# Optimization experiments

Hardware: AMD Instinct MI355X
Metric: run time of the kernel (lower is better)

Reference implementation:

```python
import jax, jax.numpy as jnp
import numpy as np

B, N, C_ATT, H, L = 4, 2048, 256, 8, 2
TOPK = 32        # torch.topk k (only index 0 per channel is used)
NSAMPLE = 32     # max_radius_points
RADIUS = 0.3
EPS = 1e-5


def _bn(x, g, b, axes):
    # training-mode batch norm (biased variance), channel dim = 1
    m = jnp.mean(x, axes, keepdims=True)
    v = jnp.var(x, axes, keepdims=True)
    sh = [1] * x.ndim
    sh[1] = -1
    return (x - m) / jnp.sqrt(v + EPS) * g.reshape(sh) + b.reshape(sh)


def _ln(x, g, b):
    m = jnp.mean(x, -1, keepdims=True)
    v = jnp.var(x, -1, keepdims=True)
    return (x - m) / jnp.sqrt(v + EPS) * g + b


def setup_inputs() -> dict:
    key = jax.random.key(0)
    ks = iter(jax.random.split(key, 40))
    def w(shape, fan):
        return jax.random.normal(next(ks), shape, jnp.float32) / np.sqrt(fan)
    return {
        "hoch_features": jax.random.normal(next(ks), (B, C_ATT, N), jnp.float32),
        "pts": jax.random.uniform(next(ks), (B, 3, N), jnp.float32),
        "Wq": w((L, C_ATT, C_ATT), C_ATT), "Wk": w((L, C_ATT, C_ATT), C_ATT),
        "Wv": w((L, C_ATT, C_ATT), C_ATT), "Wo": w((L, C_ATT, C_ATT), C_ATT),
        "ln_g": jnp.ones((L, C_ATT)), "ln_b": jnp.zeros((L, C_ATT)),
        "fg_w1": w((64, C_ATT), C_ATT), "fg_b1": jnp.zeros((64,)),
        "fg_w2": w((32, 64), 64), "fg_b2": jnp.zeros((32,)),
        "fg_w3": w((16, 32), 32), "fg_b3": jnp.zeros((16,)),
        "fg_g1": jnp.ones((64,)), "fg_be1": jnp.zeros((64,)),
        "fg_g2": jnp.ones((32,)), "fg_be2": jnp.zeros((32,)),
        "fg_g3": jnp.ones((16,)), "fg_be3": jnp.zeros((16,)),
        "cw1": w((64, 3), 3), "cw2": w((256, 64), 64), "cw3": w((512, 256), 256),
        "cg1": jnp.ones((64,)), "cb1": jnp.zeros((64,)),
        "cg2": jnp.ones((256,)), "cb2": jnp.zeros((256,)),
        "cg3": jnp.ones((512,)), "cb3": jnp.zeros((512,)),
    }


def _forward(hoch_features, pts, Wq, Wk, Wv, Wo, ln_g, ln_b,
             fg_w1, fg_b1, fg_w2, fg_b2, fg_w3, fg_b3,
             fg_g1, fg_be1, fg_g2, fg_be2, fg_g3, fg_be3,
             cw1, cw2, cw3, cg1, cb1, cg2, cb2, cg3, cb3):
    # ---- multi-head self-attention stack on (B,N,C) ----
    x = hoch_features.transpose(0, 2, 1)
    dh = C_ATT // H
    for l in range(L):
        q = (x @ Wq[l]).reshape(B, N, H, dh)
        k = (x @ Wk[l]).reshape(B, N, H, dh)
        v = (x @ Wv[l]).reshape(B, N, H, dh)
        att = jax.nn.softmax(jnp.einsum('bnhd,bmhd->bhnm', q, k) / np.sqrt(dh).astype(np.float32))
        o = jnp.einsum('bhnm,bmhd->bnhd', att, v).reshape(B, N, C_ATT) @ Wo[l]
        x = _ln(x + o, ln_g[l], ln_b[l])
    feats = x.transpose(0, 2, 1)                      # (B,256,N)
    # ---- feat_generator: 1x1 conv1d -> BN -> relu chain 256->64->32->16 ----
    h = jax.nn.relu(_bn(jnp.einsum('oc,bcn->bon', fg_w1, feats) + fg_b1[:, None], fg_g1, fg_be1, (0, 2)))
    h = jax.nn.relu(_bn(jnp.einsum('oc,bcn->bon', fg_w2, h) + fg_b2[:, None], fg_g2, fg_be2, (0, 2)))
    h = jax.nn.relu(_bn(jnp.einsum('oc,bcn->bon', fg_w3, h) + fg_b3[:, None], fg_g3, fg_be3, (0, 2)))  # (B,16,N)
    # ---- topk over points, keep argmax per channel -> 16 query points ----
    _, ti = jax.lax.top_k(h, TOPK)                    # (B,16,32)
    idx = ti[:, :, 0]                                 # (B,16)
    all_pts = pts.transpose(0, 2, 1)                  # (B,N,3)
    qpts = jax.vmap(lambda p, i: p[i])(all_pts, idx)  # (B,16,3)
    # ---- ball query (fixed-radius kNN fill, PointNet++ style) ----
    sqd = (jnp.sum(qpts * qpts, -1)[:, :, None] + jnp.sum(all_pts * all_pts, -1)[:, None, :]
           - 2.0 * jnp.einsum('bsc,bnc->bsn', qpts, all_pts))      # (B,16,N)
    gi = jnp.broadcast_to(jnp.arange(N), sqd.shape)
    gi = jnp.where(sqd > RADIUS * RADIUS, N, gi)
    gi = jnp.sort(gi, axis=-1)[:, :, :NSAMPLE]
    gi = jnp.where(gi == N, gi[:, :, :1], gi)         # (B,16,32)
    rpts = jax.vmap(lambda p, i: p[i])(all_pts, gi)   # (B,16,32,3)
    grouped = jnp.concatenate([qpts[:, :, None, :], rpts], axis=2)  # (B,16,33,3)
    g = grouped.transpose(0, 3, 1, 2)                 # (B,3,16,33)
    # ---- 1x1 conv2d -> BN2d -> LeakyReLU(0.2) chain 3->64->256->512 ----
    lrelu = lambda t: jnp.where(t > 0, t, 0.2 * t)
    g = lrelu(_bn(jnp.einsum('oc,bcsk->bosk', cw1, g), cg1, cb1, (0, 2, 3)))
    g = lrelu(_bn(jnp.einsum('oc,bcsk->bosk', cw2, g), cg2, cb2, (0, 2, 3)))
    g = lrelu(_bn(jnp.einsum('oc,bcsk->bosk', cw3, g), cg3, cb3, (0, 2, 3)))
    return jnp.max(g, axis=-1)                        # (B,512,16)


def reference(hoch_features, pts, Wq, Wk, Wv, Wo, ln_g, ln_b,
              fg_w1, fg_b1, fg_w2, fg_b2, fg_w3, fg_b3,
              fg_g1, fg_be1, fg_g2, fg_be2, fg_g3, fg_be3,
              cw1, cw2, cw3, cg1, cb1, cg2, cb2, cg3, cb3):
    return _forward(hoch_features, pts, Wq, Wk, Wv, Wo, ln_g, ln_b,
                    fg_w1, fg_b1, fg_w2, fg_b2, fg_w3, fg_b3,
                    fg_g1, fg_be1, fg_g2, fg_be2, fg_g3, fg_be3,
                    cw1, cw2, cw3, cg1, cb1, cg2, cb2, cg3, cb3)
```

## Files before the change

### kernel.cpp

```cpp
#include <hip/hip_runtime.h>
#include <hip/hip_bf16.h>
#include <math.h>

#define BB 4
#define NN 2048
#define CC 256
#define HH 8
#define DH 32
#define LL 2
#define SS 16
#define KK 33
#define NSAMPLE 32
#define EPSV 1e-5f

typedef _Float16 f16x8 __attribute__((ext_vector_type(8)));
typedef _Float16 f16x4 __attribute__((ext_vector_type(4)));
typedef float f32x4 __attribute__((ext_vector_type(4)));

struct hl16 { _Float16 h, l; };
__device__ __forceinline__ hl16 split2(float v) {
    hl16 r;
    r.h = (_Float16)v;
    r.l = (_Float16)(v - (float)r.h);
    return r;
}

#define INV_MF (1.f / 8192.f)
#define INV_MG (1.f / 2112.f)

#define WT_SLOT 65536
#define FG1H_OFF 1048576
#define FG1L_OFF (FG1H_OFF + 16384)
#define CW2H_OFF (FG1H_OFF + 32768)
#define CW2L_OFF (FG1H_OFF + 49152)
#define CW3H_OFF (FG1H_OFF + 65536)
#define CW3L_OFF (CW3H_OFF + 131072)

__global__ __launch_bounds__(256) void prep_split_k(
    const float* __restrict__ Wq, const float* __restrict__ Wk,
    const float* __restrict__ Wv, const float* __restrict__ Wo,
    const float* __restrict__ fgw1, const float* __restrict__ cw2,
    const float* __restrict__ cw3, _Float16* __restrict__ wt,
    float* __restrict__ stats0) {
    int e = blockIdx.x * 256 + threadIdx.x;
    if (e < 6144) stats0[e] = 0.f;
    if (e < 524288) {
        int slot = e >> 16;
        int l = slot >> 2, mat = slot & 3;
        int r = e & 65535;
        int n = r >> 8, k = r & 255;
        const float* W = mat == 0 ? Wq : mat == 1 ? Wk : mat == 2 ? Wv : Wo;
        hl16 s = split2(W[(size_t)l * 65536 + k * 256 + n]);
        wt[(size_t)(2 * slot) * WT_SLOT + n * 256 + k] = s.h;
        wt[(size_t)(2 * slot + 1) * WT_SLOT + n * 256 + k] = s.l;
    } else if (e < 524288 + 16384) {
        int r = e - 524288;
        hl16 s = split2(fgw1[r]);
        wt[FG1H_OFF + r] = s.h;
        wt[FG1L_OFF + r] = s.l;
    } else if (e < 524288 + 32768) {
        int r = e - (524288 + 16384);
        hl16 s = split2(cw2[r]);
        wt[CW2H_OFF + r] = s.h;
        wt[CW2L_OFF + r] = s.l;
    } else if (e < 524288 + 32768 + 131072) {
        int r = e - (524288 + 32768);
        hl16 s = split2(cw3[r]);
        wt[CW3H_OFF + r] = s.h;
        wt[CW3L_OFF + r] = s.l;
    }
}

__global__ __launch_bounds__(256) void transpose_split_k(const float* __restrict__ in,
                                                         float* __restrict__ out,
                                                         _Float16* __restrict__ oh,
                                                         _Float16* __restrict__ ol) {
    __shared__ float tls[32][33];
    int n0 = blockIdx.x * 32, c0 = blockIdx.y * 32, b = blockIdx.z;
    const float* ip = in + (size_t)b * CC * NN;
    size_t ob = (size_t)b * NN * CC;
    int tx = threadIdx.x, ty = threadIdx.y;
#pragma unroll
    for (int i = 0; i < 4; ++i)
        tls[ty + i * 8][tx] = ip[(size_t)(c0 + ty + i * 8) * NN + n0 + tx];
    __syncthreads();
#pragma unroll
    for (int i = 0; i < 4; ++i) {
        size_t oi = ob + (size_t)(n0 + ty + i * 8) * CC + c0 + tx;
        float v = tls[tx][ty + i * 8];
        out[oi] = v;
        hl16 s = split2(v);
        oh[oi] = s.h;
        ol[oi] = s.l;
    }
}

template <bool TRANSB, bool BIAS>
__global__ __launch_bounds__(256) void gemm_k(const float* __restrict__ A,
                                              const float* __restrict__ Bm,
                                              const float* __restrict__ bias,
                                              float* __restrict__ Cm,
                                              int M, int Nc, int K,
                                              const float* __restrict__ pst,
                                              const float* __restrict__ pg,
                                              const float* __restrict__ pb,
                                              float pInvM,
                                              float* __restrict__ ost) {
    __shared__ float As[16][68];
    __shared__ float Bs[16][68];
    __shared__ float sSc[64], sSh[64];
    int t = threadIdx.x;
    int tx = t & 15, ty = t >> 4;
    int row0 = blockIdx.y * 64, col0 = blockIdx.x * 64;
    if (pst && t < K) {
        float mean = pst[t] * pInvM;
        float var = pst[K + t] * pInvM - mean * mean;
        float wv = rsqrtf(var + EPSV) * pg[t];
        sSc[t] = wv;
        sSh[t] = pb[t] - mean * wv;
    }
    if (pst) __syncthreads();
    float acc[4][4] = {};
    for (int k0 = 0; k0 < K; k0 += 16) {
#pragma unroll
        for (int p = 0; p < 4; ++p) {
            int i = t + 256 * p;
            int m = i >> 4, k = i & 15;
            int gm = row0 + m, gk = k0 + k;
            float av = 0.f;
            if (gm < M && gk < K) {
                av = A[(size_t)gm * K + gk];
                if (pst) {
                    av = fmaf(av, sSc[gk], sSh[gk]);
                    av = fmaxf(av, 0.f);
                }
            }
            As[k][m] = av;
        }
#pragma unroll
        for (int p = 0; p < 4; ++p) {
            int i = t + 256 * p;
            if (TRANSB) {
                int k = i & 15, n = i >> 4;
                int gn = col0 + n, gk = k0 + k;
                Bs[k][n] = (gn < Nc && gk < K) ? Bm[(size_t)gn * K + gk] : 0.f;
            } else {
                int n = i & 63, k = i >> 6;
                int gn = col0 + n, gk = k0 + k;
                Bs[k][n] = (gn < Nc && gk < K) ? Bm[(size_t)gk * Nc + gn] : 0.f;
            }
        }
        __syncthreads();
#pragma unroll
        for (int kk = 0; kk < 16; ++kk) {
            float4 a4 = *(const float4*)&As[kk][ty * 4];
            float4 b4 = *(const float4*)&Bs[kk][tx * 4];
            float av[4] = {a4.x, a4.y, a4.z, a4.w};
            float bv[4] = {b4.x, b4.y, b4.z, b4.w};
#pragma unroll
            for (int i = 0; i < 4; ++i)
#pragma unroll
                for (int j = 0; j < 4; ++j) acc[i][j] = fmaf(av[i], bv[j], acc[i][j]);
        }
        __syncthreads();
    }
    float cs[4] = {}, css[4] = {};
#pragma unroll
    for (int i = 0; i < 4; ++i) {
        int r = row0 + ty * 4 + i;
        if (r >= M) continue;
#pragma unroll
        for (int j = 0; j < 4; ++j) {
            int c = col0 + tx * 4 + j;
            if (c >= Nc) continue;
            float v = acc[i][j];
            if (BIAS) v += bias[c];
            Cm[(size_t)r * Nc + c] = v;
            cs[j] += v;
            css[j] += v * v;
        }
    }
    if (ost) {
        float* sc = &As[0][0];
        if (t < 128) sc[t] = 0.f;
        __syncthreads();
#pragma unroll
        for (int j = 0; j < 4; ++j) {
            atomicAdd(&sc[tx * 4 + j], cs[j]);
            atomicAdd(&sc[64 + tx * 4 + j], css[j]);
        }
        __syncthreads();
        if (t < Nc) atomicAdd(&ost[t], sc[t]);
        else if (t >= 64 && t - 64 < Nc) atomicAdd(&ost[Nc + t - 64], sc[t]);
    }
}

#define EPI_F32 0
#define EPI_QK 1
#define EPI_VT 2

template <int TM>
__device__ __forceinline__ void gemm_h_body(
    const _Float16* __restrict__ Ah, const _Float16* __restrict__ Al,
    const _Float16* __restrict__ Bh, const _Float16* __restrict__ Bl,
    const float* __restrict__ bias, float* __restrict__ Cf,
    _Float16* __restrict__ Ch, _Float16* __restrict__ Cl,
    int Nc, int K, int row0, int col0, int mode, float scl,
    float* __restrict__ ost,
    _Float16* sAh, _Float16* sAl, _Float16* sBh, _Float16* sBl) {
    int t = threadIdx.x, w = t >> 6, lane = t & 63;
    int col = lane & 15, quad = lane >> 4;
    const int m0w = (TM == 128) ? (w & 1) * 64 : 0;
    const int n0w = (TM == 128) ? (w >> 1) * 32 : w * 16;
    constexpr int NT = (TM == 128) ? 2 : 1;
    constexpr int AC = TM / 64;
    f32x4 acc[4][NT];
#pragma unroll
    for (int i = 0; i < 4; ++i)
#pragma unroll
        for (int j = 0; j < NT; ++j) acc[i][j] = (f32x4){0.f, 0.f, 0.f, 0.f};

    for (int k0 = 0; k0 < K; k0 += 32) {
        f16x8 rah[AC], ral[AC], rbh, rbl;
#pragma unroll
        for (int i = 0; i < AC; ++i) {
            int idx = t + 256 * i;
            int r = idx >> 2, off = (idx & 3) * 8;
            rah[i] = *(const f16x8*)(Ah + (size_t)(row0 + r) * K + k0 + off);
            ral[i] = *(const f16x8*)(Al + (size_t)(row0 + r) * K + k0 + off);
        }
        {
            int r = t >> 2, off = (t & 3) * 8;
            rbh = *(const f16x8*)(Bh + (size_t)(col0 + r) * K + k0 + off);
            rbl = *(const f16x8*)(Bl + (size_t)(col0 + r) * K + k0 + off);
        }
        __syncthreads();
#pragma unroll
        for (int i = 0; i < AC; ++i) {
            int idx = t + 256 * i;
            int r = idx >> 2, off = (idx & 3) * 8;
            *(f16x8*)&sAh[r * 40 + off] = rah[i];
            *(f16x8*)&sAl[r * 40 + off] = ral[i];
        }
        {
            int r = t >> 2, off = (t & 3) * 8;
            *(f16x8*)&sBh[r * 40 + off] = rbh;
            *(f16x8*)&sBl[r * 40 + off] = rbl;
        }
        __syncthreads();
        f16x8 fah[4], fal[4], fbh[NT], fbl[NT];
#pragma unroll
        for (int i = 0; i < 4; ++i) {
            fah[i] = *(const f16x8*)&sAh[(m0w + i * 16 + col) * 40 + quad * 8];
            fal[i] = *(const f16x8*)&sAl[(m0w + i * 16 + col) * 40 + quad * 8];
        }
#pragma unroll
        for (int j = 0; j < NT; ++j) {
            fbh[j] = *(const f16x8*)&sBh[(n0w + j * 16 + col) * 40 + quad * 8];
            fbl[j] = *(const f16x8*)&sBl[(n0w + j * 16 + col) * 40 + quad * 8];
        }
#pragma unroll
        for (int i = 0; i < 4; ++i)
#pragma unroll
            for (int j = 0; j < NT; ++j) {
                acc[i][j] = __builtin_amdgcn_mfma_f32_16x16x32_f16(fah[i], fbh[j], acc[i][j], 0, 0, 0);
                acc[i][j] = __builtin_amdgcn_mfma_f32_16x16x32_f16(fah[i], fbl[j], acc[i][j], 0, 0, 0);
                acc[i][j] = __builtin_amdgcn_mfma_f32_16x16x32_f16(fal[i], fbh[j], acc[i][j], 0, 0, 0);
            }
    }
    float s = 0.f, ss = 0.f;
#pragma unroll
    for (int i = 0; i < 4; ++i)
#pragma unroll
        for (int j = 0; j < NT; ++j) {
            int n = col0 + n0w + j * 16 + col;
            int mb = row0 + m0w + i * 16 + quad * 4;
            if (mode == EPI_F32) {
                float bv = bias ? bias[n] : 0.f;
#pragma unroll
                for (int r = 0; r < 4; ++r) {
                    float v = acc[i][j][r] + bv;
                    Cf[(size_t)(mb + r) * Nc + n] = v;
                    s += v;
                    ss += v * v;
                }
            } else if (mode == EPI_QK) {
#pragma unroll
                for (int r = 0; r < 4; ++r) {
                    hl16 sp = split2(acc[i][j][r] * scl);
                    Ch[(size_t)(mb + r) * Nc + n] = sp.h;
                    Cl[(size_t)(mb + r) * Nc + n] = sp.l;
                }
            } else {
                int b = mb >> 11, token = mb & 2047;
                int h = n >> 5, d = n & 31;
                f16x4 h4, l4;
#pragma unroll
                for (int r = 0; r < 4; ++r) {
                    hl16 sp = split2(acc[i][j][r]);
                    h4[r] = sp.h;
                    l4[r] = sp.l;
                }
                size_t dst = ((size_t)(b * HH + h) * DH + d) * NN + token;
                *(f16x4*)&Ch[dst] = h4;
                *(f16x4*)&Cl[dst] = l4;
            }
        }
    if (ost && mode == EPI_F32 && TM == 64) {
        s += __shfl_xor(s, 16);
        s += __shfl_xor(s, 32);
        ss += __shfl_xor(ss, 16);
        ss += __shfl_xor(ss, 32);
        if (quad == 0) {
            int n = col0 + n0w + col;
            atomicAdd(&ost[n], s);
            atomicAdd(&ost[Nc + n], ss);
        }
    }
}

template <int TM>
__global__ __launch_bounds__(256) void gemm_h_k(const _Float16* __restrict__ Ah,
                                                const _Float16* __restrict__ Al,
                                                const _Float16* __restrict__ Bh,
                                                const _Float16* __restrict__ Bl,
                                                const float* __restrict__ bias,
                                                float* __restrict__ Cf, int Nc, int K,
                                                float* __restrict__ ost) {
    __shared__ _Float16 sAh[TM * 40], sAl[TM * 40], sBh[64 * 40], sBl[64 * 40];
    gemm_h_body<TM>(Ah, Al, Bh, Bl, bias, Cf, nullptr, nullptr, Nc, K,
                    blockIdx.y * TM, blockIdx.x * 64, EPI_F32, 1.f, ost,
                    sAh, sAl, sBh, sBl);
}

__global__ __launch_bounds__(256) void qkv_h_k(const _Float16* __restrict__ Xh,
                                               const _Float16* __restrict__ Xl,
                                               const _Float16* __restrict__ wt, int layer,
                                               _Float16* Qh, _Float16* Ql,
                                               _Float16* Kh, _Float16* Kl,
                                               _Float16* Vh, _Float16* Vl) {
    __shared__ _Float16 sAh[128 * 40], sAl[128 * 40], sBh[64 * 40], sBl[64 * 40];
    int mat = blockIdx.x >> 2;
    int slot = (layer * 4 + mat) * 2;
    const _Float16* Bh = wt + (size_t)slot * WT_SLOT;
    const _Float16* Bl = wt + (size_t)(slot + 1) * WT_SLOT;
    _Float16* Ch = mat == 0 ? Qh : mat == 1 ? Kh : Vh;
    _Float16* Cl = mat == 0 ? Ql : mat == 1 ? Kl : Vl;
    int mode = (mat == 2) ? EPI_VT : EPI_QK;
    float scl = (mat == 0) ? 0.25501654859214384f : 1.f;
    gemm_h_body<128>(Xh, Xl, Bh, Bl, nullptr, nullptr, Ch, Cl, CC, CC,
                     blockIdx.y * 128, (blockIdx.x & 3) * 64, mode, scl, nullptr,
                     sAh, sAl, sBh, sBl);
}

__global__ __launch_bounds__(256) void attn6_k(const _Float16* __restrict__ Qhp,
                                               const _Float16* __restrict__ Qlp,
                                               const _Float16* __restrict__ Kh,
                                               const _Float16* __restrict__ Kl,
                                               const _Float16* __restrict__ Vh,
                                               const _Float16* __restrict__ Vl,
                                               float* __restrict__ O0,
                                               float* __restrict__ O1,
                                               float* __restrict__ ML) {
    __shared__ _Float16 sKh[64 * 40], sKl[64 * 40];
    __shared__ _Float16 sVh[32 * 72], sVl[32 * 72];
    __shared__ _Float16 sPh[4][16 * 40], sPl[4][16 * 40];
    int t = threadIdx.x, w = t >> 6, lane = t & 63;
    int col = lane & 15, quad = lane >> 4;
    int bh = blockIdx.z, b = bh >> 3, h = bh & 7;
    int kh = blockIdx.y;
    int qbase = blockIdx.x * 64 + w * 16;

    size_t qoff = ((size_t)(b * NN + qbase + col)) * CC + h * DH + quad * 8;
    f16x8 qh = *(const f16x8*)(Qhp + qoff);
    f16x8 ql = *(const f16x8*)(Qlp + qoff);

    f32x4 o0 = {0.f, 0.f, 0.f, 0.f}, o1 = {0.f, 0.f, 0.f, 0.f};
    float mrun = -1e30f, lsum = 0.f;

    const _Float16* fKh = &sKh[col * 40 + quad * 8];
    const _Float16* fKl = &sKl[col * 40 + quad * 8];
    const _Float16* fVh0 = &sVh[col * 72 + quad * 8];
    const _Float16* fVl0 = &sVl[col * 72 + quad * 8];
    const _Float16* fVh1 = &sVh[(16 + col) * 72 + quad * 8];
    const _Float16* fVl1 = &sVl[(16 + col) * 72 + quad * 8];
    _Float16* wPh = &sPh[w][col * 40 + quad * 4];
    _Float16* wPl = &sPl[w][col * 40 + quad * 4];
    const _Float16* rPh = &sPh[w][col * 40 + quad * 8];
    const _Float16* rPl = &sPl[w][col * 40 + quad * 8];

    int pidx = t & 127;
    int krow = pidx >> 1, koff = (pidx & 1) * 16;
    int vrow = pidx >> 2, voff = (pidx & 3) * 16;
    const _Float16* kg = (t < 128 ? Kh : Kl) + (size_t)b * NN * CC + h * DH;
    const _Float16* vg = (t < 128 ? Vh : Vl) + ((size_t)(b * HH + h) * DH + vrow) * NN;
    _Float16* dK = (t < 128 ? sKh : sKl) + krow * 40 + koff;
    _Float16* dV = (t < 128 ? sVh : sVl) + vrow * 72 + voff;

    int kbase = kh * (NN / 2);
    for (int k0 = kbase; k0 < kbase + NN / 2; k0 += 64) {
        const _Float16* kp = kg + (size_t)(k0 + krow) * CC + koff;
        f16x8 rk0 = *(const f16x8*)kp;
        f16x8 rk1 = *(const f16x8*)(kp + 8);
        const _Float16* vp = vg + k0 + voff;
        f16x8 rv0 = *(const f16x8*)vp;
        f16x8 rv1 = *(const f16x8*)(vp + 8);
        __syncthreads();
        *(f16x8*)dK = rk0;
        *(f16x8*)(dK + 8) = rk1;
        *(f16x8*)dV = rv0;
        *(f16x8*)(dV + 8) = rv1;
        __syncthreads();

        f32x4 s[4];
#pragma unroll
        for (int kt = 0; kt < 4; ++kt) {
            f16x8 ka = *(const f16x8*)(fKh + kt * 16 * 40);
            f16x8 kb = *(const f16x8*)(fKl + kt * 16 * 40);
            f32x4 z = {0.f, 0.f, 0.f, 0.f};
            z = __builtin_amdgcn_mfma_f32_16x16x32_f16(ka, qh, z, 0, 0, 0);
            z = __builtin_amdgcn_mfma_f32_16x16x32_f16(ka, ql, z, 0, 0, 0);
            z = __builtin_amdgcn_mfma_f32_16x16x32_f16(kb, qh, z, 0, 0, 0);
            s[kt] = z;
        }

        float tm = -1e30f;
#pragma unroll
        for (int kt = 0; kt < 4; ++kt)
#pragma unroll
            for (int r = 0; r < 4; ++r) tm = fmaxf(tm, s[kt][r]);
        tm = fmaxf(tm, __shfl_xor(tm, 16));
        tm = fmaxf(tm, __shfl_xor(tm, 32));
        float nm = fmaxf(mrun, tm);
        float alpha = __builtin_amdgcn_exp2f(mrun - nm);
        float p[16], rs = 0.f;
#pragma unroll
        for (int kt = 0; kt < 4; ++kt)
#pragma unroll
            for (int r = 0; r < 4; ++r) {
                float pv = __builtin_amdgcn_exp2f(s[kt][r] - nm);
                p[kt * 4 + r] = pv;
                rs += pv;
            }
        rs += __shfl_xor(rs, 16);
        rs += __shfl_xor(rs, 32);
        lsum = lsum * alpha + rs;
        mrun = nm;
        o0.x *= alpha; o0.y *= alpha; o0.z *= alpha; o0.w *= alpha;
        o1.x *= alpha; o1.y *= alpha; o1.z *= alpha; o1.w *= alpha;

#pragma unroll
        for (int c = 0; c < 2; ++c) {
#pragma unroll
            for (int k2 = 0; k2 < 2; ++k2) {
                int kt = c * 2 + k2;
                f16x4 h4, l4;
#pragma unroll
                for (int r = 0; r < 4; ++r) {
                    hl16 sp = split2(p[kt * 4 + r]);
                    h4[r] = sp.h;
                    l4[r] = sp.l;
                }
                *(f16x4*)(wPh + k2 * 16) = h4;
                *(f16x4*)(wPl + k2 * 16) = l4;
            }
            __asm__ volatile("s_waitcnt lgkmcnt(0)" ::: "memory");
            f16x8 pH = *(const f16x8*)rPh;
            f16x8 pL = *(const f16x8*)rPl;

            f16x8 va = *(const f16x8*)(fVh0 + c * 32);
            f16x8 vb = *(const f16x8*)(fVl0 + c * 32);
            o0 = __builtin_amdgcn_mfma_f32_16x16x32_f16(va, pH, o0, 0, 0, 0);
            o0 = __builtin_amdgcn_mfma_f32_16x16x32_f16(va, pL, o0, 0, 0, 0);
            o0 = __builtin_amdgcn_mfma_f32_16x16x32_f16(vb, pH, o0, 0, 0, 0);
            f16x8 vc = *(const f16x8*)(fVh1 + c * 32);
            f16x8 vd = *(const f16x8*)(fVl1 + c * 32);
            o1 = __builtin_amdgcn_mfma_f32_16x16x32_f16(vc, pH, o1, 0, 0, 0);
            o1 = __builtin_amdgcn_mfma_f32_16x16x32_f16(vc, pL, o1, 0, 0, 0);
            o1 = __builtin_amdgcn_mfma_f32_16x16x32_f16(vd, pH, o1, 0, 0, 0);
        }
    }

    float* OP = (kh == 0) ? O0 : O1;
    int q = qbase + col;
    size_t oi = ((size_t)bh * NN + q) * 32;
    *(f32x4*)&OP[oi + quad * 4] = o0;
    *(f32x4*)&OP[oi + 16 + quad * 4] = o1;
    if (quad == 0) {
        float2* mlp = (float2*)ML;
        mlp[(size_t)kh * (BB * HH * NN) + (size_t)bh * NN + q] = make_float2(mrun, lsum);
    }
}

__global__ __launch_bounds__(256) void attn_comb_k(const float* __restrict__ O0,
                                                   const float* __restrict__ O1,
                                                   const float* __restrict__ ML,
                                                   _Float16* __restrict__ QOh,
                                                   _Float16* __restrict__ QOl) {
    int i = blockIdx.x * 256 + threadIdx.x;
    int bh = i >> 11, q = i & 2047;
    int b = bh >> 3, h = bh & 7;
    const float2* mlp = (const float2*)ML;
    float2 ml0 = mlp[i];
    float2 ml1 = mlp[BB * HH * NN + i];
    float m = fmaxf(ml0.x, ml1.x);
    float a0 = __builtin_amdgcn_exp2f(ml0.x - m);
    float a1 = __builtin_amdgcn_exp2f(ml1.x - m);
    float inv = 1.f / (ml0.y * a0 + ml1.y * a1);
    a0 *= inv;
    a1 *= inv;
    size_t src = (size_t)i * 32;
    size_t dst = ((size_t)(b * NN + q)) * CC + h * DH;
#pragma unroll
    for (int d = 0; d < 32; d += 4) {
        float4 v0 = *(const float4*)&O0[src + d];
        float4 v1 = *(const float4*)&O1[src + d];
        float vv[4] = {v0.x * a0 + v1.x * a1, v0.y * a0 + v1.y * a1,
                       v0.z * a0 + v1.z * a1, v0.w * a0 + v1.w * a1};
        f16x4 h4, l4;
#pragma unroll
        for (int r = 0; r < 4; ++r) {
            hl16 s = split2(vv[r]);
            h4[r] = s.h;
            l4[r] = s.l;
        }
        *(f16x4*)&QOh[dst + d] = h4;
        *(f16x4*)&QOl[dst + d] = l4;
    }
}

__global__ __launch_bounds__(256) void add_ln_k(float* __restrict__ X,
                                                const float* __restrict__ P,
                                                const float* __restrict__ g,
                                                const float* __restrict__ bta,
                                                _Float16* __restrict__ Xh,
                                                _Float16* __restrict__ Xl) {
    int wave = threadIdx.x >> 6, lane = threadIdx.x & 63;
    size_t row = (size_t)blockIdx.x * 4 + wave;
    size_t base = row * CC + lane * 4;
    float4 x = *(float4*)(X + base);
    float4 p = *(const float4*)(P + base);
    x.x += p.x; x.y += p.y; x.z += p.z; x.w += p.w;
    float sum = x.x + x.y + x.z + x.w;
    float ss = x.x * x.x + x.y * x.y + x.z * x.z + x.w * x.w;
#pragma unroll
    for (int off = 32; off; off >>= 1) {
        sum += __shfl_down(sum, off);
        ss += __shfl_down(ss, off);
    }
    sum = __shfl(sum, 0);
    ss = __shfl(ss, 0);
    float mean = sum * (1.f / 256.f);
    float var = ss * (1.f / 256.f) - mean * mean;
    float wn = rsqrtf(var + EPSV);
    float4 gg = *(const float4*)(g + lane * 4);
    float4 bb = *(const float4*)(bta + lane * 4);
    x.x = (x.x - mean) * wn * gg.x + bb.x;
    x.y = (x.y - mean) * wn * gg.y + bb.y;
    x.z = (x.z - mean) * wn * gg.z + bb.z;
    x.w = (x.w - mean) * wn * gg.w + bb.w;
    *(float4*)(X + base) = x;
    f16x4 h4, l4;
    float xv[4] = {x.x, x.y, x.z, x.w};
#pragma unroll
    for (int j = 0; j < 4; ++j) {
        hl16 s = split2(xv[j]);
        h4[j] = s.h;
        l4[j] = s.l;
    }
    *(f16x4*)&Xh[base] = h4;
    *(f16x4*)&Xl[base] = l4;
}

__global__ __launch_bounds__(256) void applyc_k(const float* __restrict__ in,
                                                _Float16* __restrict__ oh,
                                                _Float16* __restrict__ ol,
                                                const float* __restrict__ st,
                                                const float* __restrict__ gam,
                                                const float* __restrict__ bet,
                                                int total, int Cc, float invM) {
    int i = blockIdx.x * 256 + threadIdx.x;
    if (i >= total) return;
    int c = i % Cc;
    float mean = st[c] * invM;
    float var = st[Cc + c] * invM - mean * mean;
    float sc = rsqrtf(var + EPSV) * gam[c];
    float v = fmaf(in[i] - mean, sc, bet[c]);
    v = v > 0.f ? v : 0.2f * v;
    hl16 s = split2(v);
    oh[i] = s.h;
    ol[i] = s.l;
}

__global__ __launch_bounds__(64) void select_k(const float* __restrict__ H3,
                                               const float* __restrict__ pts,
                                               const float* __restrict__ st,
                                               const float* __restrict__ gam,
                                               const float* __restrict__ bet,
                                               float* __restrict__ G0) {
    int bs = blockIdx.x;
    int b = bs >> 4, ch = bs & 15;
    int lane = threadIdx.x;
    float mean = st[ch] * INV_MF;
    float var = st[16 + ch] * INV_MF - mean * mean;
    float sc = rsqrtf(var + EPSV) * gam[ch];
    float sh = bet[ch] - mean * sc;
    float best = -1e30f;
    int bn = 0;
    for (int n = lane; n < NN; n += 64) {
        float v = fmaf(H3[((size_t)(b * NN + n)) * 16 + ch], sc, sh);
        v = fmaxf(v, 0.f);
        if (v > best) { best = v; bn = n; }
    }
#pragma unroll
    for (int off = 32; off; off >>= 1) {
        float ov = __shfl_xor(best, off);
        int on = __shfl_xor(bn, off);
        if (ov > best || (ov == best && on < bn)) { best = ov; bn = on; }
    }
    const float* px = pts + (size_t)b * 3 * NN;
    float qx = px[bn], qy = px[NN + bn], qz = px[2 * NN + bn];
    float qq = (qx * qx + qy * qy) + qz * qz;
    __shared__ int sgi[NSAMPLE];
    const float R2 = 0.09f;
    int cnt = 0;
    for (int base = 0; base < NN && cnt < NSAMPLE; base += 64) {
        int n = base + lane;
        float x = px[n], y = px[NN + n], z = px[2 * NN + n];
        float pp = (x * x + y * y) + z * z;
        float dot = (qx * x + qy * y) + qz * z;
        float sqd = (qq + pp) - 2.f * dot;
        bool ok = !(sqd > R2);
        unsigned long long mk = __ballot(ok);
        int pos = cnt + (int)__popcll(mk & ((1ull << lane) - 1ull));
        if (ok && pos < NSAMPLE) sgi[pos] = n;
        cnt += (int)__popcll(mk);
    }
    __syncthreads();
    int g0 = sgi[0];
    if (lane >= cnt && lane < NSAMPLE) sgi[lane] = g0;
    __syncthreads();
    for (int e = lane; e < KK * 3; e += 64) {
        int k = e / 3, d = e % 3;
        int src = (k == 0) ? bn : sgi[k - 1];
        G0[((size_t)bs * KK + k) * 3 + d] = px[d * NN + src];
    }
}

__global__ __launch_bounds__(256) void maxpool_k(const float* __restrict__ G3,
                                                 const float* __restrict__ st,
                                                 const float* __restrict__ gam,
                                                 const float* __restrict__ bet,
                                                 float* __restrict__ out) {
    int i = blockIdx.x * 256 + threadIdx.x;
    if (i >= BB * 512 * SS) return;
    int o = i & 511;
    int s = (i >> 9) & 15;
    int b = i >> 13;
    float mean = st[o] * INV_MG;
    float var = st[512 + o] * INV_MG - mean * mean;
    float sc = rsqrtf(var + EPSV) * gam[o];
    float sh = bet[o] - mean * sc;
    const float* p = G3 + ((size_t)(b * SS + s) * KK) * 512 + o;
    float mx = -1e30f;
#pragma unroll
    for (int k = 0; k < KK; ++k) {
        float v = fmaf(p[(size_t)k * 512], sc, sh);
        v = v > 0.f ? v : 0.2f * v;
        mx = fmaxf(mx, v);
    }
    out[((size_t)(b * 512 + o)) * SS + s] = mx;
}

extern "C" void kernel_launch(void* const* d_in, const int* in_sizes, int n_in,
                              void* d_out, int out_size, void* d_ws, size_t ws_size,
                              hipStream_t stream) {
    const float* hoch = (const float*)d_in[0];
    const float* pts = (const float*)d_in[1];
    const float* Wq = (const float*)d_in[2];
    const float* Wk = (const float*)d_in[3];
    const float* Wv = (const float*)d_in[4];
    const float* Wo = (const float*)d_in[5];
    const float* ln_g = (const float*)d_in[6];
    const float* ln_b = (const float*)d_in[7];
    const float* fg_w1 = (const float*)d_in[8];
    const float* fg_b1 = (const float*)d_in[9];
    const float* fg_w2 = (const float*)d_in[10];
    const float* fg_b2 = (const float*)d_in[11];
    const float* fg_w3 = (const float*)d_in[12];
    const float* fg_b3 = (const float*)d_in[13];
    const float* fg_g1 = (const float*)d_in[14];
    const float* fg_be1 = (const float*)d_in[15];
    const float* fg_g2 = (const float*)d_in[16];
    const float* fg_be2 = (const float*)d_in[17];
    const float* fg_g3 = (const float*)d_in[18];
    const float* fg_be3 = (const float*)d_in[19];
    const float* cw1 = (const float*)d_in[20];
    const float* cw2 = (const float*)d_in[21];
    const float* cw3 = (const float*)d_in[22];
    const float* cg1 = (const float*)d_in[23];
    const float* cb1 = (const float*)d_in[24];
    const float* cg2 = (const float*)d_in[25];
    const float* cb2 = (const float*)d_in[26];
    const float* cg3 = (const float*)d_in[27];
    const float* cb3 = (const float*)d_in[28];
    float* out = (float*)d_out;

    float* ws = (float*)d_ws;
    const size_t M1 = (size_t)BB * NN * CC;
    float* X = ws;
    float* bA = ws + M1;
    float* bB = ws + 2 * M1;
    float* bC = ws + 3 * M1;
    _Float16* hb = (_Float16*)(ws + 4 * M1);
    _Float16* Xh = hb;
    _Float16* Xl = hb + M1;
    _Float16* Qh = hb + 2 * M1;
    _Float16* Ql = hb + 3 * M1;
    _Float16* Kh = hb + 4 * M1;
    _Float16* Kl = hb + 5 * M1;
    _Float16* Vh = hb + 6 * M1;
    _Float16* Vl = hb + 7 * M1;
    _Float16* wt = hb + 8 * M1;
    float* sm = ws + 4 * M1 + (9 * M1) / 2;
    float* st1 = sm;
    float* st2 = sm + 1024;
    float* st3 = sm + 2048;
    float* st4 = sm + 3072;
    float* st5 = sm + 4096;
    float* st6 = sm + 5120;
    float* G0 = sm + 8192;

    prep_split_k<<<2688, 256, 0, stream>>>(Wq, Wk, Wv, Wo, fg_w1, cw2, cw3, wt, sm);
    transpose_split_k<<<dim3(NN / 32, CC / 32, BB), dim3(32, 8), 0, stream>>>(hoch, X, Xh, Xl);

    const int Mrows = BB * NN;
    for (int l = 0; l < LL; ++l) {
        qkv_h_k<<<dim3(12, Mrows / 128), 256, 0, stream>>>(Xh, Xl, wt, l, Qh, Ql, Kh, Kl, Vh, Vl);
        attn6_k<<<dim3(NN / 64, 2, BB * HH), 256, 0, stream>>>(Qh, Ql, Kh, Kl, Vh, Vl, bB, bC, bA);
        attn_comb_k<<<BB * HH * NN / 256, 256, 0, stream>>>(bB, bC, bA, Qh, Ql);
        int slot = (l * 4 + 3) * 2;
        gemm_h_k<128><<<dim3(CC / 64, Mrows / 128), 256, 0, stream>>>(
            Qh, Ql, wt + (size_t)slot * WT_SLOT, wt + (size_t)(slot + 1) * WT_SLOT,
            nullptr, bA, CC, CC, nullptr);
        add_ln_k<<<Mrows / 4, 256, 0, stream>>>(X, bA, ln_g + l * CC, ln_b + l * CC, Xh, Xl);
    }

    gemm_h_k<64><<<dim3(1, Mrows / 64), 256, 0, stream>>>(Xh, Xl, wt + FG1H_OFF, wt + FG1L_OFF, fg_b1, bA, 64, 256, st1);
    gemm_k<true, true><<<dim3(1, Mrows / 64), 256, 0, stream>>>(bA, fg_w2, fg_b2, bB, Mrows, 32, 64,
                                                                st1, fg_g1, fg_be1, INV_MF, st2);
    gemm_k<true, true><<<dim3(1, Mrows / 64), 256, 0, stream>>>(bB, fg_w3, fg_b3, bC, Mrows, 16, 32,
                                                                st2, fg_g2, fg_be2, INV_MF, st3);

    select_k<<<BB * SS, 64, 0, stream>>>(bC, pts, st3, fg_g3, fg_be3, G0);

    const int Mg = BB * SS * KK;
    gemm_k<true, false><<<dim3(1, Mg / 64), 256, 0, stream>>>(G0, cw1, nullptr, bA, Mg, 64, 3,
                                                              nullptr, nullptr, nullptr, 0.f, st4);
    applyc_k<<<(Mg * 64 + 255) / 256, 256, 0, stream>>>(bA, Kh, Kl, st4, cg1, cb1, Mg * 64, 64, INV_MG);
    gemm_h_k<64><<<dim3(4, Mg / 64), 256, 0, stream>>>(Kh, Kl, wt + CW2H_OFF, wt + CW2L_OFF, nullptr, bB, 256, 64, st5);
    applyc_k<<<(Mg * 256 + 255) / 256, 256, 0, stream>>>(bB, Kh, Kl, st5, cg2, cb2, Mg * 256, 256, INV_MG);
    gemm_h_k<64><<<dim3(8, Mg / 64), 256, 0, stream>>>(Kh, Kl, wt + CW3H_OFF, wt + CW3L_OFF, nullptr, bC, 512, 256, st6);

    maxpool_k<<<(BB * 512 * SS + 255) / 256, 256, 0, stream>>>(bC, st6, cg3, cb3, out);

    (void)in_sizes; (void)n_in; (void)out_size; (void)ws_size;
}
```

Baseline: 477.2 us.

## Fuse attention split-combine into Wo GEMM and BN+LeakyReLU into conv GEMM loads

The separate attention combine kernel is removed. A new Wo GEMM kernel merges the two attention partial outputs using their max/sum statistics while loading its A tiles, then splits the result to fp16 hi/lo in shared memory. The grouped conv chain drops its applyc passes and instead uses the fp32 SIMT GEMM with BN scale/shift and LeakyReLU applied while loading A, which also fixes per-column stats offsets for grids with several column blocks. This saves kernel launches and intermediate round trips through memory. In exchange, the cw2/cw3 layers move from MFMA split-fp16 GEMMs to the slower fp32 SIMT GEMM.

Result: slower. 491.0 us (+2.9%).

```diff
diff --git a/kernel.cpp b/kernel.cpp
--- a/kernel.cpp
+++ b/kernel.cpp
@@ -31,16 +31,11 @@
 #define WT_SLOT 65536
 #define FG1H_OFF 1048576
 #define FG1L_OFF (FG1H_OFF + 16384)
-#define CW2H_OFF (FG1H_OFF + 32768)
-#define CW2L_OFF (FG1H_OFF + 49152)
-#define CW3H_OFF (FG1H_OFF + 65536)
-#define CW3L_OFF (CW3H_OFF + 131072)
 
 __global__ __launch_bounds__(256) void prep_split_k(
     const float* __restrict__ Wq, const float* __restrict__ Wk,
     const float* __restrict__ Wv, const float* __restrict__ Wo,
-    const float* __restrict__ fgw1, const float* __restrict__ cw2,
-    const float* __restrict__ cw3, _Float16* __restrict__ wt,
+    const float* __restrict__ fgw1, _Float16* __restrict__ wt,
     float* __restrict__ stats0) {
     int e = blockIdx.x * 256 + threadIdx.x;
     if (e < 6144) stats0[e] = 0.f;
@@ -58,16 +53,6 @@
         hl16 s = split2(fgw1[r]);
         wt[FG1H_OFF + r] = s.h;
         wt[FG1L_OFF + r] = s.l;
-    } else if (e < 524288 + 32768) {
-        int r = e - (524288 + 16384);
-        hl16 s = split2(cw2[r]);
-        wt[CW2H_OFF + r] = s.h;
-        wt[CW2L_OFF + r] = s.l;
-    } else if (e < 524288 + 32768 + 131072) {
-        int r = e - (524288 + 32768);
-        hl16 s = split2(cw3[r]);
-        wt[CW3H_OFF + r] = s.h;
-        wt[CW3L_OFF + r] = s.l;
     }
 }
 
@@ -104,11 +89,11 @@
                                               const float* __restrict__ pst,
                                               const float* __restrict__ pg,
                                               const float* __restrict__ pb,
-                                              float pInvM,
+                                              float pInvM, float pAlpha,
                                               float* __restrict__ ost) {
     __shared__ float As[16][68];
     __shared__ float Bs[16][68];
-    __shared__ float sSc[64], sSh[64];
+    __shared__ float sSc[256], sSh[256];
     int t = threadIdx.x;
     int tx = t & 15, ty = t >> 4;
     int row0 = blockIdx.y * 64, col0 = blockIdx.x * 64;
@@ -132,7 +117,7 @@
                 av = A[(size_t)gm * K + gk];
                 if (pst) {
                     av = fmaf(av, sSc[gk], sSh[gk]);
-                    av = fmaxf(av, 0.f);
+                    av = av > 0.f ? av : pAlpha * av;
                 }
             }
             As[k][m] = av;
@@ -190,8 +175,13 @@
             atomicAdd(&sc[64 + tx * 4 + j], css[j]);
         }
         __syncthreads();
-        if (t < Nc) atomicAdd(&ost[t], sc[t]);
-        else if (t >= 64 && t - 64 < Nc) atomicAdd(&ost[Nc + t - 64], sc[t]);
+        if (t < 64) {
+            int c = col0 + t;
+            if (c < Nc) {
+                atomicAdd(&ost[c], sc[t]);
+                atomicAdd(&ost[Nc + c], sc[64 + t]);
+            }
+        }
     }
 }
 
@@ -353,6 +343,115 @@
                      sAh, sAl, sBh, sBl);
 }
 
+__global__ __launch_bounds__(256) void gemm_wo_k(const float* __restrict__ O0,
+                                                 const float* __restrict__ O1,
+                                                 const float* __restrict__ ML,
+                                                 const _Float16* __restrict__ Bh,
+                                                 const _Float16* __restrict__ Bl,
+                                                 float* __restrict__ Cf) {
+    __shared__ _Float16 sAh[128 * 40], sAl[128 * 40], sBh[64 * 40], sBl[64 * 40];
+    int t = threadIdx.x, w = t >> 6, lane = t & 63;
+    int col = lane & 15, quad = lane >> 4;
+    int m0w = (w & 1) * 64, n0w = (w >> 1) * 32;
+    int row0 = blockIdx.y * 128, col0 = blockIdx.x * 64;
+    const float2* mlp = (const float2*)ML;
+    f32x4 acc[4][2];
+#pragma unroll
+    for (int i = 0; i < 4; ++i)
+#pragma unroll
+        for (int j = 0; j < 2; ++j) acc[i][j] = (f32x4){0.f, 0.f, 0.f, 0.f};
+
+    for (int k0 = 0; k0 < CC; k0 += 32) {
+        int h = k0 >> 5;
+        float av[2][8];
+#pragma unroll
+        for (int i = 0; i < 2; ++i) {
+            int idx = t + 256 * i;
+            int r = idx >> 2, off = (idx & 3) * 8;
+            int m = row0 + r;
+            int b = m >> 11, token = m & 2047;
+            int qi = ((b * HH + h) << 11) | token;
+            float2 ml0 = mlp[qi];
+            float2 ml1 = mlp[BB * HH * NN + qi];
+            float mm = fmaxf(ml0.x, ml1.x);
+            float a0 = __builtin_amdgcn_exp2f(ml0.x - mm);
+            float a1 = __builtin_amdgcn_exp2f(ml1.x - mm);
+            float inv = 1.f / (ml0.y * a0 + ml1.y * a1);
+            a0 *= inv;
+            a1 *= inv;
+            size_t so = (size_t)qi * 32 + off;
+            float4 p0 = *(const float4*)&O0[so];
+            float4 p0b = *(const float4*)&O0[so + 4];
+            float4 p1 = *(const float4*)&O1[so];
+            float4 p1b = *(const float4*)&O1[so + 4];
+            av[i][0] = p0.x * a0 + p1.x * a1;
+            av[i][1] = p0.y * a0 + p1.y * a1;
+            av[i][2] = p0.z * a0 + p1.z * a1;
+            av[i][3] = p0.w * a0 + p1.w * a1;
+            av[i][4] = p0b.x * a0 + p1b.x * a1;
+            av[i][5] = p0b.y * a0 + p1b.y * a1;
+            av[i][6] = p0b.z * a0 + p1b.z * a1;
+            av[i][7] = p0b.w * a0 + p1b.w * a1;
+        }
+        f16x8 rbh, rbl;
+        {
+            int r = t >> 2, off = (t & 3) * 8;
+            rbh = *(const f16x8*)(Bh + (size_t)(col0 + r) * CC + k0 + off);
+            rbl = *(const f16x8*)(Bl + (size_t)(col0 + r) * CC + k0 + off);
+        }
+        __syncthreads();
+#pragma unroll
+        for (int i = 0; i < 2; ++i) {
+            int idx = t + 256 * i;
+            int r = idx >> 2, off = (idx & 3) * 8;
+            f16x8 h8, l8;
+#pragma unroll
+            for (int j = 0; j < 8; ++j) {
+                hl16 s = split2(av[i][j]);
+                h8[j] = s.h;
+                l8[j] = s.l;
+            }
+            *(f16x8*)&sAh[r * 40 + off] = h8;
+            *(f16x8*)&sAl[r * 40 + off] = l8;
+        }
+        {
+            int r = t >> 2, off = (t & 3) * 8;
+            *(f16x8*)&sBh[r * 40 + off] = rbh;
+            *(f16x8*)&sBl[r * 40 + off] = rbl;
+        }
+        __syncthreads();
+        f16x8 fah[4], fal[4], fbh[2], fbl[2];
+#pragma unroll
+        for (int i = 0; i < 4; ++i) {
+            fah[i] = *(const f16x8*)&sAh[(m0w + i * 16 + col) * 40 + quad * 8];
+            fal[i] = *(const f16x8*)&sAl[(m0w + i * 16 + col) * 40 + quad * 8];
+        }
+#pragma unroll
+        for (int j = 0; j < 2; ++j) {
+            fbh[j] = *(const f16x8*)&sBh[(n0w + j * 16 + col) * 40 + quad * 8];
+            fbl[j] = *(const f16x8*)&sBl[(n0w + j * 16 + col) * 40 + quad * 8];
+        }
+#pragma unroll
+        for (int i = 0; i < 4; ++i)
+#pragma unroll
+            for (int j = 0; j < 2; ++j) {
+                acc[i][j] = __builtin_amdgcn_mfma_f32_16x16x32_f16(fah[i], fbh[j], acc[i][j], 0, 0, 0);
+                acc[i][j] = __builtin_amdgcn_mfma_f32_16x16x32_f16(fah[i], fbl[j], acc[i][j], 0, 0, 0);
+                acc[i][j] = __builtin_amdgcn_mfma_f32_16x16x32_f16(fal[i], fbh[j], acc[i][j], 0, 0, 0);
+            }
+    }
+#pragma unroll
+    for (int i = 0; i < 4; ++i)
+#pragma unroll
+        for (int j = 0; j < 2; ++j) {
+            int n = col0 + n0w + j * 16 + col;
+            int mb = row0 + m0w + i * 16 + quad * 4;
+#pragma unroll
+            for (int r = 0; r < 4; ++r)
+                Cf[(size_t)(mb + r) * CC + n] = acc[i][j][r];
+        }
+}
+
 __global__ __launch_bounds__(256) void attn6_k(const _Float16* __restrict__ Qhp,
                                                const _Float16* __restrict__ Qlp,
                                                const _Float16* __restrict__ Kh,
@@ -492,43 +591,6 @@
     }
 }
 
-__global__ __launch_bounds__(256) void attn_comb_k(const float* __restrict__ O0,
-                                                   const float* __restrict__ O1,
-                                                   const float* __restrict__ ML,
-                                                   _Float16* __restrict__ QOh,
-                                                   _Float16* __restrict__ QOl) {
-    int i = blockIdx.x * 256 + threadIdx.x;
-    int bh = i >> 11, q = i & 2047;
-    int b = bh >> 3, h = bh & 7;
-    const float2* mlp = (const float2*)ML;
-    float2 ml0 = mlp[i];
-    float2 ml1 = mlp[BB * HH * NN + i];
-    float m = fmaxf(ml0.x, ml1.x);
-    float a0 = __builtin_amdgcn_exp2f(ml0.x - m);
-    float a1 = __builtin_amdgcn_exp2f(ml1.x - m);
-    float inv = 1.f / (ml0.y * a0 + ml1.y * a1);
-    a0 *= inv;
-    a1 *= inv;
-    size_t src = (size_t)i * 32;
-    size_t dst = ((size_t)(b * NN + q)) * CC + h * DH;
-#pragma unroll
-    for (int d = 0; d < 32; d += 4) {
-        float4 v0 = *(const float4*)&O0[src + d];
-        float4 v1 = *(const float4*)&O1[src + d];
-        float vv[4] = {v0.x * a0 + v1.x * a1, v0.y * a0 + v1.y * a1,
-                       v0.z * a0 + v1.z * a1, v0.w * a0 + v1.w * a1};
-        f16x4 h4, l4;
-#pragma unroll
-        for (int r = 0; r < 4; ++r) {
-            hl16 s = split2(vv[r]);
-            h4[r] = s.h;
-            l4[r] = s.l;
-        }
-        *(f16x4*)&QOh[dst + d] = h4;
-        *(f16x4*)&QOl[dst + d] = l4;
-    }
-}
-
 __global__ __launch_bounds__(256) void add_ln_k(float* __restrict__ X,
                                                 const float* __restrict__ P,
                                                 const float* __restrict__ g,
@@ -570,26 +632,6 @@
     }
     *(f16x4*)&Xh[base] = h4;
     *(f16x4*)&Xl[base] = l4;
-}
-
-__global__ __launch_bounds__(256) void applyc_k(const float* __restrict__ in,
-                                                _Float16* __restrict__ oh,
-                                                _Float16* __restrict__ ol,
-                                                const float* __restrict__ st,
-                                                const float* __restrict__ gam,
-                                                const float* __restrict__ bet,
-                                                int total, int Cc, float invM) {
-    int i = blockIdx.x * 256 + threadIdx.x;
-    if (i >= total) return;
-    int c = i % Cc;
-    float mean = st[c] * invM;
-    float var = st[Cc + c] * invM - mean * mean;
-    float sc = rsqrtf(var + EPSV) * gam[c];
-    float v = fmaf(in[i] - mean, sc, bet[c]);
-    v = v > 0.f ? v : 0.2f * v;
-    hl16 s = split2(v);
-    oh[i] = s.h;
-    ol[i] = s.l;
 }
 
 __global__ __launch_bounds__(64) void select_k(const float* __restrict__ H3,
@@ -731,36 +773,35 @@
     float* st6 = sm + 5120;
     float* G0 = sm + 8192;
 
-    prep_split_k<<<2688, 256, 0, stream>>>(Wq, Wk, Wv, Wo, fg_w1, cw2, cw3, wt, sm);
+    prep_split_k<<<2112, 256, 0, stream>>>(Wq, Wk, Wv, Wo, fg_w1, wt, sm);
     transpose_split_k<<<dim3(NN / 32, CC / 32, BB), dim3(32, 8), 0, stream>>>(hoch, X, Xh, Xl);
 
     const int Mrows = BB * NN;
+    float* woOut = (float*)Qh;
     for (int l = 0; l < LL; ++l) {
         qkv_h_k<<<dim3(12, Mrows / 128), 256, 0, stream>>>(Xh, Xl, wt, l, Qh, Ql, Kh, Kl, Vh, Vl);
         attn6_k<<<dim3(NN / 64, 2, BB * HH), 256, 0, stream>>>(Qh, Ql, Kh, Kl, Vh, Vl, bB, bC, bA);
-        attn_comb_k<<<BB * HH * NN / 256, 256, 0, stream>>>(bB, bC, bA, Qh, Ql);
         int slot = (l * 4 + 3) * 2;
-        gemm_h_k<128><<<dim3(CC / 64, Mrows / 128), 256, 0, stream>>>(
-            Qh, Ql, wt + (size_t)slot * WT_SLOT, wt + (size_t)(slot + 1) * WT_SLOT,
-            nullptr, bA, CC, CC, nullptr);
-        add_ln_k<<<Mrows / 4, 256, 0, stream>>>(X, bA, ln_g + l * CC, ln_b + l * CC, Xh, Xl);
+        gemm_wo_k<<<dim3(CC / 64, Mrows / 128), 256, 0, stream>>>(
+            bB, bC, bA, wt + (size_t)slot * WT_SLOT, wt + (size_t)(slot + 1) * WT_SLOT, woOut);
+        add_ln_k<<<Mrows / 4, 256, 0, stream>>>(X, woOut, ln_g + l * CC, ln_b + l * CC, Xh, Xl);
     }
 
     gemm_h_k<64><<<dim3(1, Mrows / 64), 256, 0, stream>>>(Xh, Xl, wt + FG1H_OFF, wt + FG1L_OFF, fg_b1, bA, 64, 256, st1);
     gemm_k<true, true><<<dim3(1, Mrows / 64), 256, 0, stream>>>(bA, fg_w2, fg_b2, bB, Mrows, 32, 64,
-                                                                st1, fg_g1, fg_be1, INV_MF, st2);
+                                                                st1, fg_g1, fg_be1, INV_MF, 0.f, st2);
     gemm_k<true, true><<<dim3(1, Mrows / 64), 256, 0, stream>>>(bB, fg_w3, fg_b3, bC, Mrows, 16, 32,
-                                                                st2, fg_g2, fg_be2, INV_MF, st3);
+                                                                st2, fg_g2, fg_be2, INV_MF, 0.f, st3);
 
     select_k<<<BB * SS, 64, 0, stream>>>(bC, pts, st3, fg_g3, fg_be3, G0);
 
     const int Mg = BB * SS * KK;
     gemm_k<true, false><<<dim3(1, Mg / 64), 256, 0, stream>>>(G0, cw1, nullptr, bA, Mg, 64, 3,
-                                                              nullptr, nullptr, nullptr, 0.f, st4);
-    applyc_k<<<(Mg * 64 + 255) / 256, 256, 0, stream>>>(bA, Kh, Kl, st4, cg1, cb1, Mg * 64, 64, INV_MG);
-    gemm_h_k<64><<<dim3(4, Mg / 64), 256, 0, stream>>>(Kh, Kl, wt + CW2H_OFF, wt + CW2L_OFF, nullptr, bB, 256, 64, st5);
-    applyc_k<<<(Mg * 256 + 255) / 256, 256, 0, stream>>>(bB, Kh, Kl, st5, cg2, cb2, Mg * 256, 256, INV_MG);
-    gemm_h_k<64><<<dim3(8, Mg / 64), 256, 0, stream>>>(Kh, Kl, wt + CW3H_OFF, wt + CW3L_OFF, nullptr, bC, 512, 256, st6);
+                                                              nullptr, nullptr, nullptr, 0.f, 0.f, st4);
+    gemm_k<true, false><<<dim3(4, Mg / 64), 256, 0, stream>>>(bA, cw2, nullptr, bB, Mg, 256, 64,
+                                                              st4, cg1, cb1, INV_MG, 0.2f, st5);
+    gemm_k<true, false><<<dim3(8, Mg / 64), 256, 0, stream>>>(bB, cw3, nullptr, bC, Mg, 512, 256,
+                                                              st5, cg2, cb2, INV_MG, 0.2f, st6);
 
     maxpool_k<<<(BB * 512 * SS + 255) / 256, 256, 0, stream>>>(bC, st6, cg3, cb3, out);
 
```
